# Kernel optimization log

Hardware: AMD Instinct MI355X
Metric: run time of the kernel (lower is better)

## Reference

```python
import jax, jax.numpy as jnp
import numpy as np

DIM = 1024
H = 16
D = DIM // H
CS = 64  # chunk_size
SCALE = D ** -0.5


def setup_inputs() -> dict:
    key = jax.random.key(0)
    k1, k2, k3 = jax.random.split(key, 3)
    B, N = 4, 4096
    x = jax.random.normal(k1, (B, N, DIM), dtype=jnp.float32)
    # torch nn.Linear(dim, 3*dim, bias=False): y = x @ W.T, W:[3*dim, dim].
    # We store the transposed layout W_qkv:[dim, 3*dim] so y = x @ W_qkv.
    W_qkv = jax.random.normal(k2, (DIM, 3 * DIM), dtype=jnp.float32) * (DIM ** -0.5)
    W_out = jax.random.normal(k3, (DIM, DIM), dtype=jnp.float32) * (DIM ** -0.5)
    return {"x": x, "W_qkv": W_qkv, "W_out": W_out}


def reference(x, W_qkv, W_out):
    B, N, C = x.shape
    qkv = (x @ W_qkv).reshape(B, N, 3, H, D)
    qkv = jnp.transpose(qkv, (2, 0, 3, 1, 4))  # [3,B,H,N,D]
    q, k, v = qkv[0], qkv[1], qkv[2]
    # N chosen divisible by CS, so no padding needed (pad=0 branch).
    nc = N // CS
    q = q.reshape(B, H, nc, CS, D)
    k = k.reshape(B, H, nc, CS, D)
    v = v.reshape(B, H, nc, CS, D)
    # Local quadratic attention within each chunk, causal mask.
    attn = jnp.einsum('bhcqd,bhckd->bhcqk', q, k) * SCALE
    mask = jnp.triu(jnp.ones((CS, CS), dtype=bool), k=1)
    attn = jnp.where(mask, jnp.float32(-65000.0), attn)
    attn = jax.nn.softmax(attn, axis=-1)
    out_local = jnp.einsum('bhcqk,bhckd->bhcqd', attn, v)
    # Cross-chunk linear term (num_chunks > 1): mean-pooled K/V, exclusive cumsum.
    chunk_k = k.mean(axis=3)  # [B,H,nc,D]
    chunk_v = v.mean(axis=3)
    cum_k = jnp.cumsum(chunk_k, axis=2)
    cum_v = jnp.cumsum(chunk_v, axis=2)
    zeros = jnp.zeros((B, H, 1, D), dtype=x.dtype)
    cum_k = jnp.concatenate([zeros, cum_k[:, :, :-1]], axis=2)
    cum_v = jnp.concatenate([zeros, cum_v[:, :, :-1]], axis=2)
    cross = jax.nn.sigmoid(jnp.einsum('bhcsd,bhcd->bhcs', q, cum_k) * SCALE)
    out = out_local + cross[..., None] * cum_v[:, :, :, None, :] * 0.5
    out = out.reshape(B, H, N, D)
    out = jnp.transpose(out, (0, 2, 1, 3)).reshape(B, N, C)
    return out @ W_out
```

## Files before the change

kernel.cpp:

```cpp
#include <hip/hip_runtime.h>
#include <stdint.h>

typedef __attribute__((ext_vector_type(4))) float f32x4;
typedef __attribute__((ext_vector_type(8))) short short8;
typedef unsigned short u16;

#define NH 16
#define HD 64
#define SEQ 4096
#define BATCH 4
#define NROWS (BATCH * SEQ)
#define DIMC 1024
#define QKVC 3072
#define SCALE 0.125f

__device__ __forceinline__ u16 f2bf(float f) {
  union { float f; uint32_t u; } v; v.f = f;
  uint32_t u = v.u;
  uint32_t r = (u + 0x7fffu + ((u >> 16) & 1u)) >> 16;
  return (u16)r;
}
__device__ __forceinline__ float bf2f(u16 h) {
  union { uint32_t u; float f; } v; v.u = ((uint32_t)h) << 16;
  return v.f;
}

__global__ __launch_bounds__(256) void cvt_kernel(const float* __restrict__ in,
                                                  u16* __restrict__ out, int n4) {
  int i = blockIdx.x * 256 + threadIdx.x;
  if (i >= n4) return;
  float4 v = ((const float4*)in)[i];
  ushort4 o;
  o.x = f2bf(v.x); o.y = f2bf(v.y); o.z = f2bf(v.z); o.w = f2bf(v.w);
  ((ushort4*)out)[i] = o;
}

__global__ __launch_bounds__(256) void transpose_cvt(const float* __restrict__ in,
                                                     u16* __restrict__ out, int R, int C) {
  __shared__ float t[32][33];
  int nbx = C >> 5;
  int bx = blockIdx.x % nbx, by = blockIdx.x / nbx;
  int r0 = by << 5, c0 = bx << 5;
  int tid = threadIdx.x;
#pragma unroll
  for (int i = 0; i < 4; i++) {
    int id = i * 256 + tid; int lr = id >> 5, lc = id & 31;
    t[lr][lc] = in[(size_t)(r0 + lr) * C + (c0 + lc)];
  }
  __syncthreads();
#pragma unroll
  for (int i = 0; i < 4; i++) {
    int id = i * 256 + tid; int lr = id >> 5, lc = id & 31;
    out[(size_t)(c0 + lr) * R + (r0 + lc)] = f2bf(t[lc][lr]);
  }
}

template <int OUT_BF16>
__global__ __launch_bounds__(512, 2) void gemm_bt(const u16* __restrict__ A,
                                                  const u16* __restrict__ Bt,
                                                  void* __restrict__ Cv,
                                                  int M, int N, int K) {
  __shared__ __align__(16) u16 lds2[2][32768];
  int nbx = N >> 8;
  int nwg = gridDim.x;
  int bid = blockIdx.x;
  int cpx = nwg >> 3;
  int swz = (bid & 7) * cpx + (bid >> 3);
  int bx = swz % nbx, by = swz / nbx;
  int tid = threadIdx.x, lane = tid & 63, wv = tid >> 6;
  int wr = wv >> 2, wc = wv & 3;
  int lr = lane & 15, g = lane >> 4;
  int rx = lr & 7;
  int rsub = lane >> 3;
  int clog = (lane & 7) ^ rsub;

  const u16* Ap = A + (size_t)(by * 256) * K;
  const u16* Bp = Bt + (size_t)(bx * 256) * K;

  f32x4 acc[8][4];
#pragma unroll
  for (int m = 0; m < 8; m++)
#pragma unroll
    for (int n = 0; n < 4; n++) acc[m][n] = (f32x4){0.f, 0.f, 0.f, 0.f};

  short8 a0[4][2], a1[4][2], b0[2][2], b1[2][2];

#define ISSUE_A(HALF, L, T) do {                                                \
    int ru_ = (HALF) * 128 + (L) * 64 + wv * 8;                                 \
    const u16* g_ = Ap + (size_t)(ru_ + rsub) * K + (T) * 64 + clog * 8;        \
    __builtin_amdgcn_global_load_lds(                                           \
        (const __attribute__((address_space(1))) uint32_t*)g_,                  \
        (__attribute__((address_space(3))) uint32_t*)&lds2[(T) & 1][ru_ * 64],  \
        16, 0, 0);                                                              \
  } while (0)

#define ISSUE_B(HALF, L, T) do {                                                \
    int ru_ = (HALF) * 128 + (L) * 64 + wv * 8;                                 \
    const u16* g_ = Bp + (size_t)(ru_ + rsub) * K + (T) * 64 + clog * 8;        \
    __builtin_amdgcn_global_load_lds(                                           \
        (const __attribute__((address_space(1))) uint32_t*)g_,                  \
        (__attribute__((address_space(3)))                                      \
             uint32_t*)&lds2[(T) & 1][16384 + ru_ * 64],                        \
        16, 0, 0);                                                              \
  } while (0)

#define LDA(DST, MH, T) do {                                                    \
    _Pragma("unroll")                                                           \
    for (int m2 = 0; m2 < 4; m2++) {                                            \
      int row_ = wr * 128 + ((MH) * 4 + m2) * 16 + lr;                          \
      const u16* bp_ = &lds2[(T) & 1][row_ * 64];                               \
      _Pragma("unroll")                                                         \
      for (int s = 0; s < 2; s++)                                               \
        DST[m2][s] = *(const short8*)(bp_ + (((s * 4 + g) ^ rx) << 3));         \
    }                                                                           \
  } while (0)

#define LDB(DST, NHh, T) do {                                                   \
    _Pragma("unroll")                                                           \
    for (int n2 = 0; n2 < 2; n2++) {                                            \
      int row_ = wc * 64 + ((NHh) * 2 + n2) * 16 + lr;                          \
      const u16* bp_ = &lds2[(T) & 1][16384 + row_ * 64];                       \
      _Pragma("unroll")                                                         \
      for (int s = 0; s < 2; s++)                                               \
        DST[n2][s] = *(const short8*)(bp_ + (((s * 4 + g) ^ rx) << 3));         \
    }                                                                           \
  } while (0)

#define MFMA_Q(MH, NHh, AA, BB) do {                                            \
    _Pragma("unroll")                                                           \
    for (int s = 0; s < 2; s++)                                                 \
      _Pragma("unroll")                                                         \
      for (int m2 = 0; m2 < 4; m2++)                                            \
        _Pragma("unroll")                                                       \
        for (int n2 = 0; n2 < 2; n2++)                                          \
          acc[(MH) * 4 + m2][(NHh) * 2 + n2] =                                  \
              __builtin_amdgcn_mfma_f32_16x16x32_bf16(                          \
                  AA[m2][s], BB[n2][s], acc[(MH) * 4 + m2][(NHh) * 2 + n2],     \
                  0, 0, 0);                                                     \
  } while (0)

  int NT = K >> 6;
  ISSUE_A(0, 0, 0); ISSUE_A(0, 1, 0); ISSUE_A(1, 0, 0); ISSUE_A(1, 1, 0);
  ISSUE_B(0, 0, 0); ISSUE_B(0, 1, 0); ISSUE_B(1, 0, 0); ISSUE_B(1, 1, 0);
  __syncthreads();

  for (int t = 0; t < NT; t++) {
    LDA(a0, 0, t);
    LDB(b0, 0, t);
    __builtin_amdgcn_sched_barrier(0);
    if (t + 1 < NT) {
      ISSUE_A(0, 0, t + 1); ISSUE_A(0, 1, t + 1);
      ISSUE_A(1, 0, t + 1); ISSUE_A(1, 1, t + 1);
    }
    __builtin_amdgcn_sched_barrier(0);
    LDB(b1, 1, t);
    LDA(a1, 1, t);
    __builtin_amdgcn_sched_barrier(0);
    if (t + 1 < NT) {
      ISSUE_B(0, 0, t + 1); ISSUE_B(0, 1, t + 1);
      ISSUE_B(1, 0, t + 1); ISSUE_B(1, 1, t + 1);
    }
    __builtin_amdgcn_sched_barrier(0);
    __builtin_amdgcn_s_setprio(1);
    MFMA_Q(0, 0, a0, b0);
    __builtin_amdgcn_sched_barrier(0);
    MFMA_Q(0, 1, a0, b1);
    __builtin_amdgcn_sched_barrier(0);
    MFMA_Q(1, 1, a1, b1);
    __builtin_amdgcn_sched_barrier(0);
    MFMA_Q(1, 0, a1, b0);
    __builtin_amdgcn_s_setprio(0);
    __syncthreads();
  }

#undef ISSUE_A
#undef ISSUE_B
#undef LDA
#undef LDB
#undef MFMA_Q

  int rb = by * 256 + wr * 128, cb = bx * 256 + wc * 64;
#pragma unroll
  for (int m = 0; m < 8; m++)
#pragma unroll
    for (int n = 0; n < 4; n++)
#pragma unroll
      for (int r = 0; r < 4; r++) {
        int rg = rb + m * 16 + g * 4 + r;
        int cg = cb + n * 16 + lr;
        float v = acc[m][n][r];
        if (OUT_BF16)
          ((u16*)Cv)[(size_t)rg * N + cg] = f2bf(v);
        else
          ((float*)Cv)[(size_t)rg * N + cg] = v;
      }
}

__global__ __launch_bounds__(256) void chunk_sums(const u16* __restrict__ qkv,
                                                  float* __restrict__ ck,
                                                  float* __restrict__ cv) {
  int b = blockIdx.x >> 6, c = blockIdx.x & 63;
  int col = threadIdx.x * 4;
  const u16* base = qkv + (size_t)(b * SEQ + c * 64) * QKVC + 1024 + col;
  float sk0 = 0.f, sk1 = 0.f, sk2 = 0.f, sk3 = 0.f;
  float sv0 = 0.f, sv1 = 0.f, sv2 = 0.f, sv3 = 0.f;
#pragma unroll 8
  for (int r = 0; r < 64; r++) {
    ushort4 kk = *(const ushort4*)(base + (size_t)r * QKVC);
    ushort4 vv = *(const ushort4*)(base + (size_t)r * QKVC + 1024);
    sk0 += bf2f(kk.x); sk1 += bf2f(kk.y); sk2 += bf2f(kk.z); sk3 += bf2f(kk.w);
    sv0 += bf2f(vv.x); sv1 += bf2f(vv.y); sv2 += bf2f(vv.z); sv3 += bf2f(vv.w);
  }
  int h = col >> 6, d = col & 63;
  size_t o = (((size_t)(b * 16 + h)) * 64 + c) * 64 + d;
  ck[o]     = sk0 * 0.015625f; ck[o + 1] = sk1 * 0.015625f;
  ck[o + 2] = sk2 * 0.015625f; ck[o + 3] = sk3 * 0.015625f;
  cv[o]     = sv0 * 0.015625f; cv[o + 1] = sv1 * 0.015625f;
  cv[o + 2] = sv2 * 0.015625f; cv[o + 3] = sv3 * 0.015625f;
}

__global__ void cumsum_excl(const float* __restrict__ ck, const float* __restrict__ cv,
                            float* __restrict__ cuk, float* __restrict__ cuv) {
  int bh = blockIdx.x;
  int d = threadIdx.x;
  float ak = 0.f, av = 0.f;
  for (int c = 0; c < 64; c++) {
    size_t i = ((size_t)bh * 64 + c) * 64 + d;
    cuk[i] = ak; cuv[i] = av;
    ak += ck[i]; av += cv[i];
  }
}

__global__ __launch_bounds__(256) void attn_kernel(const u16* __restrict__ qkv,
                                                   const float* __restrict__ cuk,
                                                   const float* __restrict__ cuv,
                                                   u16* __restrict__ out) {
  int blk = blockIdx.x;
  int c = blk & 63, h = (blk >> 6) & 15, b = blk >> 10;
  int row0 = b * SEQ + c * 64;
  __shared__ u16 q_s[64][80];
  __shared__ u16 k_s[64][80];
  __shared__ u16 vt_s[64][80];
  __shared__ u16 p_s[64][80];
  __shared__ u16 ck_s[64];
  __shared__ float cv_s[64];
  int tid = threadIdx.x;
  {
    int r = tid >> 2, qt = tid & 3;
    const u16* rp = qkv + (size_t)(row0 + r) * QKVC + h * 64 + qt * 16;
    uint4 q0 = *(const uint4*)rp;          uint4 q1 = *(const uint4*)(rp + 8);
    uint4 k0 = *(const uint4*)(rp + 1024); uint4 k1 = *(const uint4*)(rp + 1032);
    uint4 v0 = *(const uint4*)(rp + 2048); uint4 v1 = *(const uint4*)(rp + 2056);
    *(uint4*)&q_s[r][qt * 16] = q0;     *(uint4*)&q_s[r][qt * 16 + 8] = q1;
    *(uint4*)&k_s[r][qt * 16] = k0;     *(uint4*)&k_s[r][qt * 16 + 8] = k1;
    const u16* vv0 = (const u16*)&v0;   const u16* vv1 = (const u16*)&v1;
#pragma unroll
    for (int j = 0; j < 8; j++) vt_s[qt * 16 + j][r] = vv0[j];
#pragma unroll
    for (int j = 0; j < 8; j++) vt_s[qt * 16 + 8 + j][r] = vv1[j];
    if (tid < 64) {
      ck_s[tid] = f2bf(cuk[(size_t)blk * 64 + tid]);
      cv_s[tid] = cuv[(size_t)blk * 64 + tid];
    }
  }
  __syncthreads();

  int lane = tid & 63, w = tid >> 6;
  int lr = lane & 15, g = lane >> 4;
  f32x4 accS[4];
#pragma unroll
  for (int n = 0; n < 4; n++) accS[n] = (f32x4){0.f, 0.f, 0.f, 0.f};
  f32x4 accC = (f32x4){0.f, 0.f, 0.f, 0.f};
  short8 zf = (short8){0, 0, 0, 0, 0, 0, 0, 0};
#pragma unroll
  for (int kt = 0; kt < 2; kt++) {
    int lk = kt * 32 + g * 8;
    short8 af = *(const short8*)&q_s[w * 16 + lr][lk];
    short8 cf = (lr == 0) ? *(const short8*)&ck_s[lk] : zf;
    accC = __builtin_amdgcn_mfma_f32_16x16x32_bf16(af, cf, accC, 0, 0, 0);
#pragma unroll
    for (int n = 0; n < 4; n++) {
      short8 bf = *(const short8*)&k_s[n * 16 + lr][lk];
      accS[n] = __builtin_amdgcn_mfma_f32_16x16x32_bf16(af, bf, accS[n], 0, 0, 0);
    }
  }
  float crossv[4];
#pragma unroll
  for (int r4 = 0; r4 < 4; r4++) {
    int row = w * 16 + g * 4 + r4;
    float x[4];
    float mx = -3.4e38f;
#pragma unroll
    for (int n = 0; n < 4; n++) {
      int col = n * 16 + lr;
      x[n] = ((col & 63) > (row & 63)) ? -65000.0f : accS[n][r4] * SCALE;
      mx = fmaxf(mx, x[n]);
    }
    mx = fmaxf(mx, __shfl_xor(mx, 1));
    mx = fmaxf(mx, __shfl_xor(mx, 2));
    mx = fmaxf(mx, __shfl_xor(mx, 4));
    mx = fmaxf(mx, __shfl_xor(mx, 8));
    float p[4], sum = 0.f;
#pragma unroll
    for (int n = 0; n < 4; n++) { p[n] = __expf(x[n] - mx); sum += p[n]; }
    sum += __shfl_xor(sum, 1);
    sum += __shfl_xor(sum, 2);
    sum += __shfl_xor(sum, 4);
    sum += __shfl_xor(sum, 8);
    float inv = 1.0f / sum;
#pragma unroll
    for (int n = 0; n < 4; n++) p_s[row][n * 16 + lr] = f2bf(p[n] * inv);
    float sg = 1.0f / (1.0f + __expf(-accC[r4] * SCALE));
    crossv[r4] = __shfl(sg, (lane & 48));
  }
  __syncthreads();
  f32x4 accO[4];
#pragma unroll
  for (int n = 0; n < 4; n++) accO[n] = (f32x4){0.f, 0.f, 0.f, 0.f};
#pragma unroll
  for (int kt = 0; kt < 2; kt++) {
    int lk = kt * 32 + g * 8;
    short8 pf = *(const short8*)&p_s[w * 16 + lr][lk];
#pragma unroll
    for (int n = 0; n < 4; n++) {
      short8 vf = *(const short8*)&vt_s[n * 16 + lr][lk];
      accO[n] = __builtin_amdgcn_mfma_f32_16x16x32_bf16(pf, vf, accO[n], 0, 0, 0);
    }
  }
#pragma unroll
  for (int n = 0; n < 4; n++)
#pragma unroll
    for (int r4 = 0; r4 < 4; r4++) {
      int row = w * 16 + g * 4 + r4;
      int col = n * 16 + lr;
      float v = accO[n][r4] + crossv[r4] * cv_s[col] * 0.5f;
      out[(size_t)(row0 + row) * DIMC + h * 64 + col] = f2bf(v);
    }
}

extern "C" void kernel_launch(void* const* d_in, const int* in_sizes, int n_in,
                              void* d_out, int out_size, void* d_ws, size_t ws_size,
                              hipStream_t stream) {
  const float* x = (const float*)d_in[0];
  const float* Wqkv = (const float*)d_in[1];
  const float* Wout = (const float*)d_in[2];
  char* ws = (char*)d_ws;
  size_t off = 0;
  auto alloc = [&](size_t b) {
    void* p = ws + off;
    off += (b + 255) & ~(size_t)255;
    return p;
  };
  u16* xb = (u16*)alloc((size_t)NROWS * DIMC * 2);
  u16* wqt = (u16*)alloc((size_t)QKVC * DIMC * 2);
  u16* wot = (u16*)alloc((size_t)DIMC * DIMC * 2);
  u16* qkvb = (u16*)alloc((size_t)NROWS * QKVC * 2);
  float* chk = (float*)alloc((size_t)4096 * 64 * 4);
  float* chv = (float*)alloc((size_t)4096 * 64 * 4);
  float* cuk = (float*)alloc((size_t)4096 * 64 * 4);
  float* cuv = (float*)alloc((size_t)4096 * 64 * 4);
  u16* attnb = xb;

  cvt_kernel<<<16384, 256, 0, stream>>>(x, xb, NROWS * DIMC / 4);
  transpose_cvt<<<3072, 256, 0, stream>>>(Wqkv, wqt, DIMC, QKVC);
  transpose_cvt<<<1024, 256, 0, stream>>>(Wout, wot, DIMC, DIMC);
  gemm_bt<1><<<768, 512, 0, stream>>>(xb, wqt, qkvb, NROWS, QKVC, DIMC);
  chunk_sums<<<256, 256, 0, stream>>>(qkvb, chk, chv);
  cumsum_excl<<<64, 64, 0, stream>>>(chk, chv, cuk, cuv);
  attn_kernel<<<4096, 256, 0, stream>>>(qkvb, cuk, cuv, attnb);
  gemm_bt<0><<<256, 512, 0, stream>>>(attnb, wot, d_out, NROWS, DIMC, DIMC);
}
```

Baseline: 214.1 us.

## Interleave LDS reads with MFMA in GEMM and fuse chunk sums into epilogue

```diff
diff --git a/kernel.cpp b/kernel.cpp
--- a/kernel.cpp
+++ b/kernel.cpp
@@ -55,10 +55,12 @@
   }
 }
 
-template <int OUT_BF16>
+template <int OUT_BF16, int DO_SUMS>
 __global__ __launch_bounds__(512, 2) void gemm_bt(const u16* __restrict__ A,
                                                   const u16* __restrict__ Bt,
                                                   void* __restrict__ Cv,
+                                                  float* __restrict__ chk,
+                                                  float* __restrict__ chv,
                                                   int M, int N, int K) {
   __shared__ __align__(16) u16 lds2[2][32768];
   int nbx = N >> 8;
@@ -142,35 +144,51 @@
   int NT = K >> 6;
   ISSUE_A(0, 0, 0); ISSUE_A(0, 1, 0); ISSUE_A(1, 0, 0); ISSUE_A(1, 1, 0);
   ISSUE_B(0, 0, 0); ISSUE_B(0, 1, 0); ISSUE_B(1, 0, 0); ISSUE_B(1, 1, 0);
-  __syncthreads();
+  asm volatile("s_waitcnt vmcnt(0)" ::: "memory");
+  __builtin_amdgcn_s_barrier();
+  LDA(a0, 0, 0);
+  LDB(b0, 0, 0);
+  __builtin_amdgcn_sched_barrier(0);
 
   for (int t = 0; t < NT; t++) {
-    LDA(a0, 0, t);
-    LDB(b0, 0, t);
-    __builtin_amdgcn_sched_barrier(0);
+    LDB(b1, 1, t);
     if (t + 1 < NT) {
       ISSUE_A(0, 0, t + 1); ISSUE_A(0, 1, t + 1);
       ISSUE_A(1, 0, t + 1); ISSUE_A(1, 1, t + 1);
     }
     __builtin_amdgcn_sched_barrier(0);
-    LDB(b1, 1, t);
+    __builtin_amdgcn_s_setprio(1);
+    MFMA_Q(0, 0, a0, b0);
+    __builtin_amdgcn_s_setprio(0);
+    __builtin_amdgcn_sched_barrier(0);
+    __builtin_amdgcn_s_barrier();
     LDA(a1, 1, t);
-    __builtin_amdgcn_sched_barrier(0);
     if (t + 1 < NT) {
       ISSUE_B(0, 0, t + 1); ISSUE_B(0, 1, t + 1);
       ISSUE_B(1, 0, t + 1); ISSUE_B(1, 1, t + 1);
     }
     __builtin_amdgcn_sched_barrier(0);
     __builtin_amdgcn_s_setprio(1);
-    MFMA_Q(0, 0, a0, b0);
-    __builtin_amdgcn_sched_barrier(0);
     MFMA_Q(0, 1, a0, b1);
-    __builtin_amdgcn_sched_barrier(0);
-    MFMA_Q(1, 1, a1, b1);
-    __builtin_amdgcn_sched_barrier(0);
+    __builtin_amdgcn_s_setprio(0);
+    __builtin_amdgcn_sched_barrier(0);
+    __builtin_amdgcn_s_barrier();
+    __builtin_amdgcn_s_setprio(1);
     MFMA_Q(1, 0, a1, b0);
     __builtin_amdgcn_s_setprio(0);
-    __syncthreads();
+    __builtin_amdgcn_sched_barrier(0);
+    asm volatile("s_waitcnt vmcnt(0)" ::: "memory");
+    __builtin_amdgcn_s_barrier();
+    if (t + 1 < NT) {
+      LDA(a0, 0, t + 1);
+      LDB(b0, 0, t + 1);
+    }
+    __builtin_amdgcn_sched_barrier(0);
+    __builtin_amdgcn_s_setprio(1);
+    MFMA_Q(1, 1, a1, b1);
+    __builtin_amdgcn_s_setprio(0);
+    __builtin_amdgcn_sched_barrier(0);
+    __builtin_amdgcn_s_barrier();
   }
 
 #undef ISSUE_A
@@ -180,6 +198,31 @@
 #undef MFMA_Q
 
   int rb = by * 256 + wr * 128, cb = bx * 256 + wc * 64;
+
+  if (DO_SUMS && cb >= 1024) {
+#pragma unroll
+    for (int mh = 0; mh < 2; mh++)
+#pragma unroll
+      for (int n = 0; n < 4; n++) {
+        float sum = 0.f;
+#pragma unroll
+        for (int m = mh * 4; m < mh * 4 + 4; m++)
+#pragma unroll
+          for (int r = 0; r < 4; r++) sum += acc[m][n][r];
+        sum += __shfl_xor(sum, 16);
+        sum += __shfl_xor(sum, 32);
+        if (g == 0) {
+          int grb = rb + mh * 64;
+          int b = grb >> 12, c = (grb >> 6) & 63;
+          int cg = cb + n * 16 + lr;
+          int col = cg & 1023;
+          int h = col >> 6, d = col & 63;
+          float* dst = (cg < 2048) ? chk : chv;
+          dst[(((size_t)(b * 16 + h)) * 64 + c) * 64 + d] = sum * 0.015625f;
+        }
+      }
+  }
+
 #pragma unroll
   for (int m = 0; m < 8; m++)
 #pragma unroll
@@ -194,29 +237,6 @@
         else
           ((float*)Cv)[(size_t)rg * N + cg] = v;
       }
-}
-
-__global__ __launch_bounds__(256) void chunk_sums(const u16* __restrict__ qkv,
-                                                  float* __restrict__ ck,
-                                                  float* __restrict__ cv) {
-  int b = blockIdx.x >> 6, c = blockIdx.x & 63;
-  int col = threadIdx.x * 4;
-  const u16* base = qkv + (size_t)(b * SEQ + c * 64) * QKVC + 1024 + col;
-  float sk0 = 0.f, sk1 = 0.f, sk2 = 0.f, sk3 = 0.f;
-  float sv0 = 0.f, sv1 = 0.f, sv2 = 0.f, sv3 = 0.f;
-#pragma unroll 8
-  for (int r = 0; r < 64; r++) {
-    ushort4 kk = *(const ushort4*)(base + (size_t)r * QKVC);
-    ushort4 vv = *(const ushort4*)(base + (size_t)r * QKVC + 1024);
-    sk0 += bf2f(kk.x); sk1 += bf2f(kk.y); sk2 += bf2f(kk.z); sk3 += bf2f(kk.w);
-    sv0 += bf2f(vv.x); sv1 += bf2f(vv.y); sv2 += bf2f(vv.z); sv3 += bf2f(vv.w);
-  }
-  int h = col >> 6, d = col & 63;
-  size_t o = (((size_t)(b * 16 + h)) * 64 + c) * 64 + d;
-  ck[o]     = sk0 * 0.015625f; ck[o + 1] = sk1 * 0.015625f;
-  ck[o + 2] = sk2 * 0.015625f; ck[o + 3] = sk3 * 0.015625f;
-  cv[o]     = sv0 * 0.015625f; cv[o + 1] = sv1 * 0.015625f;
-  cv[o + 2] = sv2 * 0.015625f; cv[o + 3] = sv3 * 0.015625f;
 }
 
 __global__ void cumsum_excl(const float* __restrict__ ck, const float* __restrict__ cv,
@@ -364,9 +384,9 @@
   cvt_kernel<<<16384, 256, 0, stream>>>(x, xb, NROWS * DIMC / 4);
   transpose_cvt<<<3072, 256, 0, stream>>>(Wqkv, wqt, DIMC, QKVC);
   transpose_cvt<<<1024, 256, 0, stream>>>(Wout, wot, DIMC, DIMC);
-  gemm_bt<1><<<768, 512, 0, stream>>>(xb, wqt, qkvb, NROWS, QKVC, DIMC);
-  chunk_sums<<<256, 256, 0, stream>>>(qkvb, chk, chv);
+  gemm_bt<1, 1><<<768, 512, 0, stream>>>(xb, wqt, qkvb, chk, chv, NROWS, QKVC, DIMC);
   cumsum_excl<<<64, 64, 0, stream>>>(chk, chv, cuk, cuv);
   attn_kernel<<<4096, 256, 0, stream>>>(qkvb, cuk, cuv, attnb);
-  gemm_bt<0><<<256, 512, 0, stream>>>(attnb, wot, d_out, NROWS, DIMC, DIMC);
-}
+  gemm_bt<0, 0><<<256, 512, 0, stream>>>(attnb, wot, d_out, nullptr, nullptr,
+                                         NROWS, DIMC, DIMC);
+}
```

After: 203.5 us. 1.05x faster.
